# Performance work log

Measured on AMD Instinct MI355X. Metric: run time of the kernel, lower is better.

## Reference

```python
import jax, jax.numpy as jnp
import numpy as np

B, S, D, H = 2, 2048, 1024, 16
HEAD_DIM = D // H
WINDOW = 256
DILATION = 1
NEG = jnp.float32(-1e9)


def _build_attn_mask(seq_len):
    # Faithful port of torch _build_attn_mask for causal=True, stencil kind='local'.
    idx = jnp.arange(seq_len)
    diff = idx[None, :] - idx[:, None]  # diff[i, j] = j - i (torch diff is idx.unsqueeze(0)-idx.unsqueeze(1))
    # causal: -inf strictly above diagonal (j > i)
    mask = jnp.where(diff > 0, -jnp.inf, 0.0).astype(jnp.float32)
    # stencil allow: |diff| <= window and |diff| % dilation == 0
    cond = (jnp.abs(diff) <= WINDOW) & (jnp.abs(diff) % DILATION == 0)
    allowed = jnp.where(cond, 0.0, -jnp.inf).astype(jnp.float32)
    # torch.maximum: allow() can UNMASK causally-masked positions inside the window
    mask = jnp.maximum(mask, allowed)
    # clamp(min=-1e9)
    return jnp.maximum(mask, NEG)


def setup_inputs() -> dict:
    key = jax.random.key(0)
    k = jax.random.split(key, 5)
    return {
        "x": jax.random.normal(k[0], (B, S, D), dtype=jnp.float32),
        "in_proj_w": jax.random.normal(k[1], (3 * D, D), dtype=jnp.float32) * (D ** -0.5),
        "in_proj_b": jax.random.normal(k[2], (3 * D,), dtype=jnp.float32) * 0.02,
        "out_proj_w": jax.random.normal(k[3], (D, D), dtype=jnp.float32) * (D ** -0.5),
        "out_proj_b": jax.random.normal(k[4], (D,), dtype=jnp.float32) * 0.02,
    }


def reference(x, in_proj_w, in_proj_b, out_proj_w, out_proj_b):
    b, s, d = x.shape
    # fused qkv projection (torch nn.MultiheadAttention in_proj)
    qkv = x @ in_proj_w.T + in_proj_b  # [b, s, 3d]
    q, k, v = jnp.split(qkv, 3, axis=-1)

    def to_heads(t):
        return t.reshape(b, s, H, HEAD_DIM).transpose(0, 2, 1, 3)  # [b, h, s, hd]

    q, k, v = to_heads(q), to_heads(k), to_heads(v)
    scale = jnp.float32(HEAD_DIM) ** -0.5
    scores = jnp.einsum("bhqd,bhkd->bhqk", q * scale, k)  # [b, h, s, s]
    mask = _build_attn_mask(s)  # [s, s]
    scores = scores + mask[None, None, :, :]
    attn = jax.nn.softmax(scores, axis=-1)
    out = jnp.einsum("bhqk,bhkd->bhqd", attn, v)  # [b, h, s, hd]
    out = out.transpose(0, 2, 1, 3).reshape(b, s, d)
    return out @ out_proj_w.T + out_proj_b
```

## Files before the change

### kernel.cpp

```cpp
#include <hip/hip_runtime.h>
#include <cstddef>

#define BATCH   2
#define SEQ     2048
#define DMODEL  1024
#define NH      16
#define HDIM    64
#define WIN     256
#define MTOT    4096

typedef __bf16 bf16;
typedef __attribute__((ext_vector_type(8)))  __bf16 bf16x8;
typedef __attribute__((ext_vector_type(4)))  float  f32x4;
typedef __attribute__((ext_vector_type(16))) float  f32x16;

#define GLOAD_LDS(gp, lp) __builtin_amdgcn_global_load_lds( \
    (const __attribute__((address_space(1))) void*)(gp),    \
    (__attribute__((address_space(3))) void*)(lp), 16, 0, 0)

__device__ __forceinline__ float fast_exp2(float x) {
#if __has_builtin(__builtin_amdgcn_exp2f)
  return __builtin_amdgcn_exp2f(x);
#else
  float r; asm("v_exp_f32 %0, %1" : "=v"(r) : "v"(x)); return r;
#endif
}

__device__ __forceinline__ unsigned int cvtpk_bf16(float lo, float hi) {
  unsigned int r;
  asm("v_cvt_pk_bf16_f32 %0, %1, %2" : "=v"(r) : "v"(lo), "v"(hi));
  return r;
}

__global__ __launch_bounds__(256)
void cvt_all(const float* __restrict__ x, const float* __restrict__ w1,
             const float* __restrict__ w2, bf16* __restrict__ xh,
             bf16* __restrict__ xl, bf16* __restrict__ w1h,
             bf16* __restrict__ w1l, bf16* __restrict__ w2h,
             bf16* __restrict__ w2l) {
  const int bid = blockIdx.x;
  const float* s; bf16 *hp, *lp; int base;
  if (bid < 2048)      { s = x;  hp = xh;  lp = xl;  base = bid * 2048; }
  else if (bid < 3584) { s = w1; hp = w1h; lp = w1l; base = (bid - 2048) * 2048; }
  else                 { s = w2; hp = w2h; lp = w2l; base = (bid - 3584) * 2048; }
  const int i = base + threadIdx.x * 8;
  float4 a = *(const float4*)(s + i);
  float4 c = *(const float4*)(s + i + 4);
  const float f[8] = {a.x, a.y, a.z, a.w, c.x, c.y, c.z, c.w};
  bf16x8 vh, vl;
#pragma unroll
  for (int j = 0; j < 8; ++j) {
    bf16 hh = (bf16)f[j];
    vh[j] = hh;
    vl[j] = (bf16)(f[j] - (float)hh);
  }
  *(bf16x8*)(hp + i) = vh;
  *(bf16x8*)(lp + i) = vl;
}

__global__ __launch_bounds__(256, 4)
void gemm_qkv_fused(const bf16* __restrict__ xh, const bf16* __restrict__ xl,
                    const bf16* __restrict__ w1h, const bf16* __restrict__ w1l,
                    const float* __restrict__ b1,
                    bf16* __restrict__ Qh, bf16* __restrict__ Ql,
                    bf16* __restrict__ Kt, bf16* __restrict__ Vt) {
  __shared__ bf16 sAh[128 * 32];
  __shared__ bf16 sAl[128 * 32];
  __shared__ bf16 sBh[128 * 32];
  __shared__ bf16 sBl[64 * 32];

  const int t = threadIdx.x, w = t >> 6, lane = t & 63;
  const int ln15 = lane & 15, quad = lane >> 4;
  const int drow = lane >> 2;
  const int dkcol = (lane & 3) * 8;
  const int bid = blockIdx.x;

  if (bid < 512) {
    const int g = bid & 7, s = bid >> 3;
    const int bm = (g * 4 + (s >> 4)) * 128;
    const int bn = (s & 15) * 64;

    f32x4 acc[2][4];
#pragma unroll
    for (int i = 0; i < 2; ++i)
#pragma unroll
      for (int j = 0; j < 4; ++j)
#pragma unroll
        for (int r = 0; r < 4; ++r) acc[i][j][r] = 0.f;

    for (int k0 = 0; k0 < DMODEL; k0 += 32) {
      __syncthreads();
#pragma unroll
      for (int half = 0; half < 2; ++half) {
        const int r = w * 32 + half * 16 + drow;
        const size_t goffA = (size_t)(bm + r) * DMODEL + k0 + dkcol;
        const int loff = (w * 32 + half * 16) * 32;
        GLOAD_LDS(xh + goffA, sAh + loff);
        GLOAD_LDS(xl + goffA, sAl + loff);
      }
      {
        const int r = w * 16 + drow;
        const size_t goffB = (size_t)(bn + r) * DMODEL + k0 + dkcol;
        const int loff = (w * 16) * 32;
        GLOAD_LDS(w1h + goffB, sBh + loff);
        GLOAD_LDS(w1l + goffB, sBl + loff);
      }
      __syncthreads();

      bf16x8 afh[2], afl[2], bfh[4], bfl[4];
#pragma unroll
      for (int mt = 0; mt < 2; ++mt) {
        const int off = (w * 32 + mt * 16 + ln15) * 32 + quad * 8;
        afh[mt] = *(const bf16x8*)&sAh[off];
        afl[mt] = *(const bf16x8*)&sAl[off];
      }
#pragma unroll
      for (int nt = 0; nt < 4; ++nt) {
        const int off = (nt * 16 + ln15) * 32 + quad * 8;
        bfh[nt] = *(const bf16x8*)&sBh[off];
        bfl[nt] = *(const bf16x8*)&sBl[off];
      }
#pragma unroll
      for (int mt = 0; mt < 2; ++mt)
#pragma unroll
        for (int nt = 0; nt < 4; ++nt) {
          acc[mt][nt] = __builtin_amdgcn_mfma_f32_16x16x32_bf16(afh[mt], bfh[nt], acc[mt][nt], 0, 0, 0);
          acc[mt][nt] = __builtin_amdgcn_mfma_f32_16x16x32_bf16(afh[mt], bfl[nt], acc[mt][nt], 0, 0, 0);
          acc[mt][nt] = __builtin_amdgcn_mfma_f32_16x16x32_bf16(afl[mt], bfh[nt], acc[mt][nt], 0, 0, 0);
        }
    }

    float bbcol[4];
#pragma unroll
    for (int nt = 0; nt < 4; ++nt) bbcol[nt] = b1[bn + nt * 16 + ln15];

#pragma unroll
    for (int mt = 0; mt < 2; ++mt)
#pragma unroll
      for (int r = 0; r < 4; ++r) {
        const size_t grow = (size_t)(bm + w * 32 + mt * 16 + quad * 4 + r);
#pragma unroll
        for (int nt = 0; nt < 4; ++nt) {
          const int col = bn + nt * 16 + ln15;
          const float v = acc[mt][nt][r] + bbcol[nt];
          const bf16 hh = (bf16)v;
          Qh[grow * 1024 + col] = hh;
          Ql[grow * 1024 + col] = (bf16)(v - (float)hh);
        }
      }
  } else if (bid < 768) {
    const int kid = bid - 512;
    const int g = kid & 7, s = kid >> 3;
    const int bm = (g * 4 + (s >> 3)) * 128;
    const int bn = 1024 + (s & 7) * 128;
    const int wrow = (w & 1) * 64, wcol = (w >> 1) * 64;

    f32x4 acc[4][4];
#pragma unroll
    for (int i = 0; i < 4; ++i)
#pragma unroll
      for (int j = 0; j < 4; ++j)
#pragma unroll
        for (int r = 0; r < 4; ++r) acc[i][j][r] = 0.f;

    for (int k0 = 0; k0 < DMODEL; k0 += 32) {
      __syncthreads();
#pragma unroll
      for (int half = 0; half < 2; ++half) {
        const int r = w * 32 + half * 16 + drow;
        const int loff = (w * 32 + half * 16) * 32;
        GLOAD_LDS(xh + (size_t)(bm + r) * DMODEL + k0 + dkcol, sAh + loff);
        GLOAD_LDS(w1h + (size_t)(bn + r) * DMODEL + k0 + dkcol, sBh + loff);
      }
      __syncthreads();

      bf16x8 af[4], bf[4];
#pragma unroll
      for (int mt = 0; mt < 4; ++mt)
        af[mt] = *(const bf16x8*)&sAh[(wrow + mt * 16 + ln15) * 32 + quad * 8];
#pragma unroll
      for (int nt = 0; nt < 4; ++nt)
        bf[nt] = *(const bf16x8*)&sBh[(wcol + nt * 16 + ln15) * 32 + quad * 8];
#pragma unroll
      for (int mt = 0; mt < 4; ++mt)
#pragma unroll
        for (int nt = 0; nt < 4; ++nt)
          acc[mt][nt] = __builtin_amdgcn_mfma_f32_16x16x32_bf16(af[mt], bf[nt], acc[mt][nt], 0, 0, 0);
    }

    float bbcol[4];
#pragma unroll
    for (int nt = 0; nt < 4; ++nt) bbcol[nt] = b1[bn + wcol + nt * 16 + ln15];

#pragma unroll
    for (int mt = 0; mt < 4; ++mt)
#pragma unroll
      for (int r = 0; r < 4; ++r) {
        const size_t grow = (size_t)(bm + wrow + mt * 16 + quad * 4 + r);
        const int btok = (int)(grow >> 11), key = (int)(grow & 2047);
        const int kt = key >> 6, kw = key & 63;
#pragma unroll
        for (int nt = 0; nt < 4; ++nt) {
          const int col = bn + wcol + nt * 16 + ln15;
          const float v = acc[mt][nt][r] + bbcol[nt];
          const int hh2 = (col - 1024) >> 6, d = col & 63;
          const size_t addr = ((size_t)((btok * 16 + hh2) * 32 + kt) << 12)
                            + (((kw >> 5) * 4 + (d >> 4)) << 9)
                            + ((((d >> 3) & 1) << 5) + (kw & 31)) * 8 + (d & 7);
          Kt[addr] = (bf16)v;
        }
      }
  } else {
    const int vid = bid - 768;
    const int bm = (vid >> 5) * 128, bn = (vid & 31) * 128;
    const int wrow = (w & 1) * 64, wcol = (w >> 1) * 64;
    const bf16* Ah = w1h + 2048 * 1024;
    const float* bias = b1 + 2048;

    f32x4 acc[4][4];
#pragma unroll
    for (int i = 0; i < 4; ++i)
#pragma unroll
      for (int j = 0; j < 4; ++j)
#pragma unroll
        for (int r = 0; r < 4; ++r) acc[i][j][r] = 0.f;

    for (int k0 = 0; k0 < DMODEL; k0 += 32) {
      __syncthreads();
#pragma unroll
      for (int half = 0; half < 2; ++half) {
        const int r = w * 32 + half * 16 + drow;
        const int loff = (w * 32 + half * 16) * 32;
        GLOAD_LDS(Ah + (size_t)(bm + r) * DMODEL + k0 + dkcol, sAh + loff);
        GLOAD_LDS(xh + (size_t)(bn + r) * DMODEL + k0 + dkcol, sBh + loff);
      }
      __syncthreads();

      bf16x8 af[4], bf[4];
#pragma unroll
      for (int mt = 0; mt < 4; ++mt)
        af[mt] = *(const bf16x8*)&sAh[(wrow + mt * 16 + ln15) * 32 + quad * 8];
#pragma unroll
      for (int nt = 0; nt < 4; ++nt)
        bf[nt] = *(const bf16x8*)&sBh[(wcol + nt * 16 + ln15) * 32 + quad * 8];
#pragma unroll
      for (int mt = 0; mt < 4; ++mt)
#pragma unroll
        for (int nt = 0; nt < 4; ++nt)
          acc[mt][nt] = __builtin_amdgcn_mfma_f32_16x16x32_bf16(af[mt], bf[nt], acc[mt][nt], 0, 0, 0);
    }

#pragma unroll
    for (int mt = 0; mt < 4; ++mt)
#pragma unroll
      for (int r = 0; r < 4; ++r) {
        const size_t grow = (size_t)(bm + wrow + mt * 16 + quad * 4 + r);
        const float brow = bias[grow];
        const int hh2 = (int)(grow >> 6), d = (int)(grow & 63);
#pragma unroll
        for (int nt = 0; nt < 4; ++nt) {
          const int col = bn + wcol + nt * 16 + ln15;
          const float v = acc[mt][nt][r] + brow;
          const int btok = col >> 11, key = col & 2047;
          const int kt = key >> 6, kw = key & 63;
          const size_t addr = ((size_t)((btok * 16 + hh2) * 32 + kt) << 12)
                            + (((d >> 5) * 4 + (kw >> 4)) << 9)
                            + ((((kw >> 3) & 1) << 5) + (d & 31)) * 8 + (kw & 7);
          Vt[addr] = (bf16)v;
        }
      }
  }
}

__global__ __launch_bounds__(256)
void gemm_out64(const bf16* __restrict__ Ah, const bf16* __restrict__ Al,
                const bf16* __restrict__ Bh, const bf16* __restrict__ Bl,
                const float* __restrict__ bias, float* __restrict__ Cf) {
  __shared__ bf16 sAh[64 * 32];
  __shared__ bf16 sAl[64 * 32];
  __shared__ bf16 sBh[64 * 32];
  __shared__ bf16 sBl[64 * 32];

  const int t = threadIdx.x, w = t >> 6, lane = t & 63;
  const int ln15 = lane & 15, quad = lane >> 4;
  const int bid = blockIdx.x;
  const int g = bid & 7, s = bid >> 3;
  const int bm = (g * 8 + (s >> 4)) * 64;
  const int bn = (s & 15) * 64;
  const int wrow = (w & 1) * 32, wcol = (w >> 1) * 32;
  const int drow = lane >> 2;
  const int dkcol = (lane & 3) * 8;

  f32x4 acc[2][2];
#pragma unroll
  for (int i = 0; i < 2; ++i)
#pragma unroll
    for (int j = 0; j < 2; ++j)
#pragma unroll
      for (int r = 0; r < 4; ++r) acc[i][j][r] = 0.f;

  for (int k0 = 0; k0 < DMODEL; k0 += 32) {
    __syncthreads();
    {
      const int r = w * 16 + drow;
      const size_t goffA = (size_t)(bm + r) * DMODEL + k0 + dkcol;
      const size_t goffB = (size_t)(bn + r) * DMODEL + k0 + dkcol;
      const int loff = (w * 16) * 32;
      GLOAD_LDS(Ah + goffA, sAh + loff);
      GLOAD_LDS(Al + goffA, sAl + loff);
      GLOAD_LDS(Bh + goffB, sBh + loff);
      GLOAD_LDS(Bl + goffB, sBl + loff);
    }
    __syncthreads();

    bf16x8 afh[2], afl[2], bfh[2], bfl[2];
#pragma unroll
    for (int mt = 0; mt < 2; ++mt) {
      const int off = (wrow + mt * 16 + ln15) * 32 + quad * 8;
      afh[mt] = *(const bf16x8*)&sAh[off];
      afl[mt] = *(const bf16x8*)&sAl[off];
    }
#pragma unroll
    for (int nt = 0; nt < 2; ++nt) {
      const int off = (wcol + nt * 16 + ln15) * 32 + quad * 8;
      bfh[nt] = *(const bf16x8*)&sBh[off];
      bfl[nt] = *(const bf16x8*)&sBl[off];
    }
#pragma unroll
    for (int mt = 0; mt < 2; ++mt)
#pragma unroll
      for (int nt = 0; nt < 2; ++nt) {
        acc[mt][nt] = __builtin_amdgcn_mfma_f32_16x16x32_bf16(afh[mt], bfh[nt], acc[mt][nt], 0, 0, 0);
        acc[mt][nt] = __builtin_amdgcn_mfma_f32_16x16x32_bf16(afh[mt], bfl[nt], acc[mt][nt], 0, 0, 0);
        acc[mt][nt] = __builtin_amdgcn_mfma_f32_16x16x32_bf16(afl[mt], bfh[nt], acc[mt][nt], 0, 0, 0);
      }
  }

  float bbcol[2];
#pragma unroll
  for (int nt = 0; nt < 2; ++nt) bbcol[nt] = bias[bn + wcol + nt * 16 + ln15];

#pragma unroll
  for (int mt = 0; mt < 2; ++mt)
#pragma unroll
    for (int r = 0; r < 4; ++r) {
      const size_t grow = (size_t)(bm + wrow + mt * 16 + quad * 4 + r);
#pragma unroll
      for (int nt = 0; nt < 2; ++nt) {
        const int col = bn + wcol + nt * 16 + ln15;
        Cf[grow * 1024 + col] = acc[mt][nt][r] + bbcol[nt];
      }
    }
}

__global__ __launch_bounds__(64, 2)
void attn_mfma(const bf16* __restrict__ Qh, const bf16* __restrict__ Ql,
               const bf16* __restrict__ Kt, const bf16* __restrict__ Vt,
               bf16* __restrict__ Omh, bf16* __restrict__ Oml) {
  const int lane = threadIdx.x & 63;
  const int ln31 = lane & 31, half = lane >> 5;
  const int bid = blockIdx.x;
  const int j = bid & 31;
  const int bh = ((j & 7) << 2) | (j >> 3);
  const int c  = 63 - (bid >> 5);
  const int b = bh >> 4, h = bh & 15;
  const int i0w = c * 32;
  const int lim = i0w + WIN;

  bf16x8 qh[4], ql[4];
  {
    const size_t rowQ = (size_t)(b * SEQ + i0w + ln31);
#pragma unroll
    for (int ks = 0; ks < 4; ++ks) {
      bf16x8 vh = *(const bf16x8*)(Qh + rowQ * 1024 + h * 64 + ks * 16 + half * 8);
      bf16x8 vl = *(const bf16x8*)(Ql + rowQ * 1024 + h * 64 + ks * 16 + half * 8);
#pragma unroll
      for (int jj = 0; jj < 8; ++jj) {
        float f = ((float)vh[jj] + (float)vl[jj]) * 0.1803368801111204f;
        bf16 hh = (bf16)f;
        qh[ks][jj] = hh;
        ql[ks][jj] = (bf16)(f - (float)hh);
      }
    }
  }

  f32x16 accO0, accO1;
#pragma unroll
  for (int r = 0; r < 16; ++r) { accO0[r] = 0.f; accO1[r] = 0.f; }
  float lsum = 0.f;

  const bf16* KtBH = Kt + ((size_t)(b * 16 + h) << 17);
  const bf16* VtBH = Vt + ((size_t)(b * 16 + h) << 17);
  const int lane8 = lane * 8;

  const int nkt = min((i0w + 31 + WIN) / 64 + 1, SEQ / 64);

  for (int kt = 0; kt < nkt; ++kt) {
    const bf16* Kb = KtBH + ((size_t)kt << 12);
    const bf16* Vb = VtBH + ((size_t)kt << 12);

    bf16x8 kf[8], vf[8];
#pragma unroll
    for (int s = 0; s < 8; ++s) {
      kf[s] = *(const bf16x8*)&Kb[(s << 9) + lane8];
      vf[s] = *(const bf16x8*)&Vb[(s << 9) + lane8];
    }

    f32x16 S0, S1;
#pragma unroll
    for (int r = 0; r < 16; ++r) { S0[r] = 0.f; S1[r] = 0.f; }
    __builtin_amdgcn_s_setprio(1);
#pragma unroll
    for (int ks = 0; ks < 4; ++ks) {
      S0 = __builtin_amdgcn_mfma_f32_32x32x16_bf16(kf[ks], qh[ks], S0, 0, 0, 0);
      S0 = __builtin_amdgcn_mfma_f32_32x32x16_bf16(kf[ks], ql[ks], S0, 0, 0, 0);
      S1 = __builtin_amdgcn_mfma_f32_32x32x16_bf16(kf[4 + ks], qh[ks], S1, 0, 0, 0);
      S1 = __builtin_amdgcn_mfma_f32_32x32x16_bf16(kf[4 + ks], ql[ks], S1, 0, 0, 0);
    }
    __builtin_amdgcn_s_setprio(0);

    const int j0 = kt * 64;
    bf16x8 pa[4];
#pragma unroll
    for (int cc = 0; cc < 2; ++cc) {
      f32x16& S = cc ? S1 : S0;
      const int base = j0 + cc * 32 - lim;
      const bool may = (base + 31 > 0);
#pragma unroll
      for (int r = 0; r < 16; ++r) {
        const int kr = (r & 3) + 8 * (r >> 2) + 4 * half;
        float pv = fast_exp2(S[r]);
        if (may && (kr + base > ln31)) pv = 0.f;
        S[r] = pv;
        lsum += pv;
      }
      unsigned int W0[4], W1[4];
#pragma unroll
      for (int g = 0; g < 4; ++g) {
        W0[g] = cvtpk_bf16(S[4 * g + 0], S[4 * g + 1]);
        W1[g] = cvtpk_bf16(S[4 * g + 2], S[4 * g + 3]);
      }
#pragma unroll
      for (int f = 0; f < 2; ++f) {
        auto s0 = __builtin_amdgcn_permlane32_swap(W0[2 * f], W0[2 * f + 1], false, false);
        auto s1 = __builtin_amdgcn_permlane32_swap(W1[2 * f], W1[2 * f + 1], false, false);
        union { unsigned int w[4]; bf16x8 v; } u;
        u.w[0] = (unsigned int)s0[0];
        u.w[1] = (unsigned int)s1[0];
        u.w[2] = (unsigned int)s0[1];
        u.w[3] = (unsigned int)s1[1];
        pa[cc * 2 + f] = u.v;
      }
    }

    __builtin_amdgcn_s_setprio(1);
#pragma unroll
    for (int ks = 0; ks < 4; ++ks) {
      accO0 = __builtin_amdgcn_mfma_f32_32x32x16_bf16(pa[ks], vf[ks], accO0, 0, 0, 0);
      accO1 = __builtin_amdgcn_mfma_f32_32x32x16_bf16(pa[ks], vf[4 + ks], accO1, 0, 0, 0);
    }
    __builtin_amdgcn_s_setprio(0);
  }

  lsum += __shfl_xor(lsum, 32, 64);
#pragma unroll
  for (int r = 0; r < 16; ++r) {
    const int rl = (r & 3) + 8 * (r >> 2) + 4 * half;
    const float lv = __shfl(lsum, rl, 64);
    const float inv = 1.0f / lv;
    const size_t grow = (size_t)(b * SEQ + i0w + rl);
    const int col0 = h * 64 + ln31;
    const float v0 = accO0[r] * inv;
    const float v1 = accO1[r] * inv;
    const bf16 h0 = (bf16)v0, h1 = (bf16)v1;
    Omh[grow * DMODEL + col0]      = h0;
    Oml[grow * DMODEL + col0]      = (bf16)(v0 - (float)h0);
    Omh[grow * DMODEL + col0 + 32] = h1;
    Oml[grow * DMODEL + col0 + 32] = (bf16)(v1 - (float)h1);
  }
}

extern "C" void kernel_launch(void* const* d_in, const int* in_sizes, int n_in,
                              void* d_out, int out_size, void* d_ws, size_t ws_size,
                              hipStream_t stream) {
  const float* x  = (const float*)d_in[0];
  const float* w1 = (const float*)d_in[1];
  const float* b1 = (const float*)d_in[2];
  const float* w2 = (const float*)d_in[3];
  const float* b2 = (const float*)d_in[4];
  float* out = (float*)d_out;

  char* ws = (char*)d_ws;
  bf16* Qh   = (bf16*)(ws + 0);
  bf16* Ql   = (bf16*)(ws + 8388608);
  bf16* Kt   = (bf16*)(ws + 16777216);
  bf16* Vt   = (bf16*)(ws + 25165824);
  bf16* xh   = (bf16*)(ws + 33554432);
  bf16* xl   = (bf16*)(ws + 41943040);
  bf16* w1h  = (bf16*)(ws + 50331648);
  bf16* w1l  = (bf16*)(ws + 56623104);
  bf16* w2h  = (bf16*)(ws + 62914560);
  bf16* w2l  = (bf16*)(ws + 65011712);
  bf16* Omh  = xh;
  bf16* Oml  = xl;

  cvt_all<<<dim3(4096), 256, 0, stream>>>(x, w1, w2, xh, xl, w1h, w1l, w2h, w2l);

  gemm_qkv_fused<<<dim3(1024), 256, 0, stream>>>(
      xh, xl, w1h, w1l, b1, Qh, Ql, Kt, Vt);

  attn_mfma<<<dim3(2048), 64, 0, stream>>>(Qh, Ql, Kt, Vt, Omh, Oml);

  gemm_out64<<<dim3(1024), 256, 0, stream>>>(
      Omh, Oml, w2h, w2l, b2, out);
}
```

Before: 222.8 us.

## Prefetch next K/V tiles in attention loop and widen out-proj K-step with swizzle

The attention loop now loads the next key tile right after the QK MFMAs and the next value tile after the PV MFMAs, so global load latency overlaps compute instead of stalling at each iteration start. Scheduling barriers pin the load placement. Separately, the output projection GEMM stages 64-wide K slices into LDS with an XOR swizzle, which halves the number of sync rounds and is meant to avoid bank conflicts. The cost is higher register pressure in attention and doubled LDS use in the GEMM.

```diff
diff --git a/kernel.cpp b/kernel.cpp
--- a/kernel.cpp
+++ b/kernel.cpp
@@ -276,10 +276,10 @@
 void gemm_out64(const bf16* __restrict__ Ah, const bf16* __restrict__ Al,
                 const bf16* __restrict__ Bh, const bf16* __restrict__ Bl,
                 const float* __restrict__ bias, float* __restrict__ Cf) {
-  __shared__ bf16 sAh[64 * 32];
-  __shared__ bf16 sAl[64 * 32];
-  __shared__ bf16 sBh[64 * 32];
-  __shared__ bf16 sBl[64 * 32];
+  __shared__ bf16 sAh[64 * 64];
+  __shared__ bf16 sAl[64 * 64];
+  __shared__ bf16 sBh[64 * 64];
+  __shared__ bf16 sBl[64 * 64];
 
   const int t = threadIdx.x, w = t >> 6, lane = t & 63;
   const int ln15 = lane & 15, quad = lane >> 4;
@@ -288,8 +288,8 @@
   const int bm = (g * 8 + (s >> 4)) * 64;
   const int bn = (s & 15) * 64;
   const int wrow = (w & 1) * 32, wcol = (w >> 1) * 32;
-  const int drow = lane >> 2;
-  const int dkcol = (lane & 3) * 8;
+  const int drow8 = lane >> 3;
+  const int dcol8 = (((lane & 7) * 8) ^ ((drow8 & 1) << 5));
 
   f32x4 acc[2][2];
 #pragma unroll
@@ -299,13 +299,14 @@
 #pragma unroll
       for (int r = 0; r < 4; ++r) acc[i][j][r] = 0.f;
 
-  for (int k0 = 0; k0 < DMODEL; k0 += 32) {
+  for (int k0 = 0; k0 < DMODEL; k0 += 64) {
     __syncthreads();
-    {
-      const int r = w * 16 + drow;
-      const size_t goffA = (size_t)(bm + r) * DMODEL + k0 + dkcol;
-      const size_t goffB = (size_t)(bn + r) * DMODEL + k0 + dkcol;
-      const int loff = (w * 16) * 32;
+#pragma unroll
+    for (int p = 0; p < 2; ++p) {
+      const int r = w * 16 + p * 8 + drow8;
+      const size_t goffA = (size_t)(bm + r) * DMODEL + k0 + dcol8;
+      const size_t goffB = (size_t)(bn + r) * DMODEL + k0 + dcol8;
+      const int loff = (w * 16 + p * 8) * 64;
       GLOAD_LDS(Ah + goffA, sAh + loff);
       GLOAD_LDS(Al + goffA, sAl + loff);
       GLOAD_LDS(Bh + goffB, sBh + loff);
@@ -313,27 +314,32 @@
     }
     __syncthreads();
 
-    bf16x8 afh[2], afl[2], bfh[2], bfl[2];
-#pragma unroll
-    for (int mt = 0; mt < 2; ++mt) {
-      const int off = (wrow + mt * 16 + ln15) * 32 + quad * 8;
-      afh[mt] = *(const bf16x8*)&sAh[off];
-      afl[mt] = *(const bf16x8*)&sAl[off];
-    }
-#pragma unroll
-    for (int nt = 0; nt < 2; ++nt) {
-      const int off = (wcol + nt * 16 + ln15) * 32 + quad * 8;
-      bfh[nt] = *(const bf16x8*)&sBh[off];
-      bfl[nt] = *(const bf16x8*)&sBl[off];
-    }
-#pragma unroll
-    for (int mt = 0; mt < 2; ++mt)
+#pragma unroll
+    for (int ks = 0; ks < 2; ++ks) {
+      bf16x8 afh[2], afl[2], bfh[2], bfl[2];
+#pragma unroll
+      for (int mt = 0; mt < 2; ++mt) {
+        const int row = wrow + mt * 16 + ln15;
+        const int off = row * 64 + ((ks * 32 + quad * 8) ^ ((row & 1) << 5));
+        afh[mt] = *(const bf16x8*)&sAh[off];
+        afl[mt] = *(const bf16x8*)&sAl[off];
+      }
 #pragma unroll
       for (int nt = 0; nt < 2; ++nt) {
-        acc[mt][nt] = __builtin_amdgcn_mfma_f32_16x16x32_bf16(afh[mt], bfh[nt], acc[mt][nt], 0, 0, 0);
-        acc[mt][nt] = __builtin_amdgcn_mfma_f32_16x16x32_bf16(afh[mt], bfl[nt], acc[mt][nt], 0, 0, 0);
-        acc[mt][nt] = __builtin_amdgcn_mfma_f32_16x16x32_bf16(afl[mt], bfh[nt], acc[mt][nt], 0, 0, 0);
-      }
+        const int row = wcol + nt * 16 + ln15;
+        const int off = row * 64 + ((ks * 32 + quad * 8) ^ ((row & 1) << 5));
+        bfh[nt] = *(const bf16x8*)&sBh[off];
+        bfl[nt] = *(const bf16x8*)&sBl[off];
+      }
+#pragma unroll
+      for (int mt = 0; mt < 2; ++mt)
+#pragma unroll
+        for (int nt = 0; nt < 2; ++nt) {
+          acc[mt][nt] = __builtin_amdgcn_mfma_f32_16x16x32_bf16(afh[mt], bfh[nt], acc[mt][nt], 0, 0, 0);
+          acc[mt][nt] = __builtin_amdgcn_mfma_f32_16x16x32_bf16(afh[mt], bfl[nt], acc[mt][nt], 0, 0, 0);
+          acc[mt][nt] = __builtin_amdgcn_mfma_f32_16x16x32_bf16(afl[mt], bfh[nt], acc[mt][nt], 0, 0, 0);
+        }
+    }
   }
 
   float bbcol[2];
@@ -395,17 +401,14 @@
 
   const int nkt = min((i0w + 31 + WIN) / 64 + 1, SEQ / 64);
 
+  bf16x8 kf[8], vf[8];
+#pragma unroll
+  for (int s = 0; s < 8; ++s) {
+    kf[s] = *(const bf16x8*)&KtBH[(s << 9) + lane8];
+    vf[s] = *(const bf16x8*)&VtBH[(s << 9) + lane8];
+  }
+
   for (int kt = 0; kt < nkt; ++kt) {
-    const bf16* Kb = KtBH + ((size_t)kt << 12);
-    const bf16* Vb = VtBH + ((size_t)kt << 12);
-
-    bf16x8 kf[8], vf[8];
-#pragma unroll
-    for (int s = 0; s < 8; ++s) {
-      kf[s] = *(const bf16x8*)&Kb[(s << 9) + lane8];
-      vf[s] = *(const bf16x8*)&Vb[(s << 9) + lane8];
-    }
-
     f32x16 S0, S1;
 #pragma unroll
     for (int r = 0; r < 16; ++r) { S0[r] = 0.f; S1[r] = 0.f; }
@@ -418,6 +421,14 @@
       S1 = __builtin_amdgcn_mfma_f32_32x32x16_bf16(kf[4 + ks], ql[ks], S1, 0, 0, 0);
     }
     __builtin_amdgcn_s_setprio(0);
+
+    const int ktn = (kt + 1 < nkt) ? kt + 1 : kt;
+    const bf16* Kbn = KtBH + ((size_t)ktn << 12);
+    const bf16* Vbn = VtBH + ((size_t)ktn << 12);
+    bf16x8 kfn[8];
+#pragma unroll
+    for (int s = 0; s < 8; ++s) kfn[s] = *(const bf16x8*)&Kbn[(s << 9) + lane8];
+    __builtin_amdgcn_sched_barrier(0);
 
     const int j0 = kt * 64;
     bf16x8 pa[4];
@@ -460,6 +471,14 @@
       accO1 = __builtin_amdgcn_mfma_f32_32x32x16_bf16(pa[ks], vf[4 + ks], accO1, 0, 0, 0);
     }
     __builtin_amdgcn_s_setprio(0);
+
+    bf16x8 vfn[8];
+#pragma unroll
+    for (int s = 0; s < 8; ++s) vfn[s] = *(const bf16x8*)&Vbn[(s << 9) + lane8];
+    __builtin_amdgcn_sched_barrier(0);
+
+#pragma unroll
+    for (int s = 0; s < 8; ++s) { kf[s] = kfn[s]; vf[s] = vfn[s]; }
   }
 
   lsum += __shfl_xor(lsum, 32, 64);
```

New measurement: 242.3 us. 8.7% more time.
